# Optimization experiments

Hardware: AMD Instinct MI355X
Metric: run time of the kernel (lower is better)

## Reference

```python
import jax, jax.numpy as jnp
import numpy as np
from jax import lax

E = 1024      # embed_dim
H = 16        # num_heads
HD = E // H   # head_dim = 64
GS = 2        # head_group_size
G = H // GS   # num head groups = 8
KQ = 3        # kq kernel q size
KK = 3        # kq kernel k size


def setup_inputs() -> dict:
    key = jax.random.key(0)
    ks = jax.random.split(key, 18)
    B, S = 2, 1024
    def rn(k, shape, scale=1.0):
        return jax.random.normal(k, shape, dtype=jnp.float32) * scale
    return {
        "Q": rn(ks[0], (B, S, E)),
        "K": rn(ks[1], (B, S, E)),
        "V": rn(ks[2], (B, S, E)),
        "Wq": rn(ks[3], (E, E), 0.02), "bq": rn(ks[4], (E,), 0.02),
        "Wk": rn(ks[5], (E, E), 0.02), "bk": rn(ks[6], (E,), 0.02),
        "Wv": rn(ks[7], (E, E), 0.02), "bv": rn(ks[8], (E,), 0.02),
        "Wo": rn(ks[9], (E, E), 0.02), "bo": rn(ks[10], (E,), 0.02),
        # depthwise key-query conv: [out=H, in/groups=1, KQ, KK]
        "kq_w": rn(ks[11], (H, 1, KQ, KK), 0.1),
        "kq_b": rn(ks[12], (H,), 0.02),
        # grouped 1x1 head-mix conv: weight [H, GS] (kernel dim squeezed), bias [H]
        "mix_w": rn(ks[13], (H, GS), 0.3),
        "mix_b": rn(ks[14], (H,), 0.02),
        # DynamicTanh params over head_dim (channels_last)
        "dyt_alpha": jnp.array([0.5], dtype=jnp.float32),
        "dyt_w": jnp.ones((HD,), dtype=jnp.float32),
        "dyt_b": jnp.zeros((HD,), dtype=jnp.float32),
        "depth_scale": jnp.ones((1,), dtype=jnp.float32),
    }


def reference(Q, K, V, Wq, bq, Wk, bk, Wv, bv, Wo, bo,
              kq_w, kq_b, mix_w, mix_b, dyt_alpha, dyt_w, dyt_b, depth_scale):
    B, S, _ = Q.shape
    scale = HD ** (-0.5)
    # projections -> [B, H, S, HD]
    q = (Q @ Wq + bq).reshape(B, S, H, HD).transpose(0, 2, 1, 3)
    k = (K @ Wk + bk).reshape(B, S, H, HD).transpose(0, 2, 1, 3)
    v = (V @ Wv + bv).reshape(B, S, H, HD).transpose(0, 2, 1, 3)

    # raw logits [B, H, Sq, Sk], multiplicative causal mask (zeros above diag)
    logits = jnp.einsum('bhqd,bhkd->bhqk', q, k) * scale
    causal = jnp.tril(jnp.ones((S, S), dtype=logits.dtype))
    logits = logits * causal

    # per-head (depthwise) key-query conv2d; torch pads q-dim by 2 both sides
    # then crops to first S rows (causal in q), k-dim padded symmetrically by 1
    conv = lax.conv_general_dilated(
        logits, kq_w, window_strides=(1, 1),
        padding=[(KQ - 1, KQ - 1), ((KK - 1) // 2, (KK - 1) // 2)],
        dimension_numbers=('NCHW', 'OIHW', 'NCHW'),
        feature_group_count=H)
    conv = conv + kq_b[None, :, None, None]
    conv = conv[:, :, :S, :]

    attn = jax.nn.softmax(conv, axis=-1)

    # grouped 1x1 head-mixing conv (within groups of GS heads) + bias
    attn_g = attn.reshape(B, G, GS, S, S)
    mw = mix_w.reshape(G, GS, GS)  # [group, out_in_group, in_in_group]
    mixed = jnp.einsum('goj,bgjqk->bgoqk', mw, attn_g).reshape(B, H, S, S)
    mixed = mixed + mix_b[None, :, None, None]

    out = jnp.einsum('bhqk,bhkd->bhqd', mixed, v)
    # DynamicTanh over head_dim (channels_last) + depth scale
    out = jnp.tanh(dyt_alpha * out) * dyt_w + dyt_b
    out = out * depth_scale
    out = out.transpose(0, 2, 1, 3).reshape(B, S, E)
    return out @ Wo + bo
```

## Files before the change

### kernel.cpp

```cpp
#include <hip/hip_runtime.h>
#include <cstdint>
#include <cstddef>

typedef __bf16 bf16;
typedef __bf16 bf16x8 __attribute__((ext_vector_type(8)));
typedef float f32x4 __attribute__((ext_vector_type(4)));

#define DEVI static __device__ __forceinline__

DEVI unsigned int cvt_pk_bf16(float lo, float hi) {
  unsigned int bl = __float_as_uint(lo);
  bl += 0x7fffu + ((bl >> 16) & 1u);
  unsigned int bh = __float_as_uint(hi);
  bh += 0x7fffu + ((bh >> 16) & 1u);
  return (bl >> 16) | (bh & 0xffff0000u);
}
DEVI float bf_lo(unsigned int u) { return __uint_as_float(u << 16); }
DEVI float bf_hi(unsigned int u) { return __uint_as_float(u & 0xffff0000u); }

DEVI void gload16(const bf16* g, bf16* l) {
  __builtin_amdgcn_global_load_lds(
      (const __attribute__((address_space(1))) unsigned int*)g,
      (__attribute__((address_space(3))) unsigned int*)l, 16, 0, 0);
}

__global__ __launch_bounds__(256) void wtr_k(
    const float* __restrict__ Wq, const float* __restrict__ Wk,
    const float* __restrict__ Wv, const float* __restrict__ Wo,
    bf16* __restrict__ Wt)
{
  const int z = blockIdx.z;
  const float* W = (z == 0) ? Wq : (z == 1) ? Wk : (z == 2) ? Wv : Wo;
  bf16* out = Wt + ((size_t)z << 20);
  const int n0 = blockIdx.x * 64, k0 = blockIdx.y * 64;
  __shared__ bf16 Ts[64 * 72];
  const int tid = threadIdx.x;
  #pragma unroll
  for (int i = 0; i < 4; ++i) {
    int t = tid + i * 256;
    int kr = t >> 4, nc = t & 15;
    float4 v = *(const float4*)(W + (size_t)(k0 + kr) * 1024 + n0 + nc * 4);
    Ts[(nc * 4 + 0) * 72 + kr] = (bf16)v.x;
    Ts[(nc * 4 + 1) * 72 + kr] = (bf16)v.y;
    Ts[(nc * 4 + 2) * 72 + kr] = (bf16)v.z;
    Ts[(nc * 4 + 3) * 72 + kr] = (bf16)v.w;
  }
  __syncthreads();
  const int n = tid >> 2, kc = tid & 3;
  *(uint4*)(out + (size_t)(n0 + n) * 1024 + k0 + kc * 16) =
      *(const uint4*)(&Ts[n * 72 + kc * 16]);
  *(uint4*)(out + (size_t)(n0 + n) * 1024 + k0 + kc * 16 + 8) =
      *(const uint4*)(&Ts[n * 72 + kc * 16 + 8]);
}

__global__ __launch_bounds__(256) void a2bf_k(
    const float* __restrict__ Q, const float* __restrict__ K,
    const float* __restrict__ V, bf16* __restrict__ Ab)
{
  const int z = blockIdx.y;
  const float* A = (z == 0) ? Q : (z == 1) ? K : V;
  bf16* o = Ab + ((size_t)z << 21);
  const int idx = blockIdx.x * 256 + threadIdx.x;
  const float4 v0 = *(const float4*)(A + (size_t)idx * 8);
  const float4 v1 = *(const float4*)(A + (size_t)idx * 8 + 4);
  uint4 u;
  u.x = cvt_pk_bf16(v0.x, v0.y);
  u.y = cvt_pk_bf16(v0.z, v0.w);
  u.z = cvt_pk_bf16(v1.x, v1.y);
  u.w = cvt_pk_bf16(v1.z, v1.w);
  *(uint4*)(o + (size_t)idx * 8) = u;
}

__global__ __launch_bounds__(256) void proj_gemm_k(
    const bf16* __restrict__ Ab, const bf16* __restrict__ Wt,
    const float* __restrict__ bq, const float* __restrict__ bk,
    const float* __restrict__ bv, bf16* __restrict__ outbase)
{
  const int z = blockIdx.z;
  const bf16* A  = Ab + ((size_t)z << 21);
  const bf16* Bt = Wt + ((size_t)z << 20);
  const float* bias = (z == 0) ? bq : (z == 1) ? bk : bv;
  bf16* outb = outbase + ((size_t)z << 21);

  __shared__ __align__(16) bf16 As[2][4096];
  __shared__ __align__(16) bf16 Bs[2][2048];

  const int tid = threadIdx.x, lane = tid & 63, wid = tid >> 6;
  const int q4 = lane >> 4, n16 = lane & 15;
  const int wm = wid >> 1, wn = wid & 1;
  const int bid = blockIdx.x;
  const int m0 = (bid & 15) * 128, n0 = (bid >> 4) * 64;

  const int cA0 = wid * 64 + lane, cA1 = cA0 + 256;
  const bf16* gA0 = A + (size_t)(m0 + (cA0 >> 2)) * 1024 + (((cA0 & 3) ^ ((cA0 >> 3) & 3)) << 3);
  const bf16* gA1 = A + (size_t)(m0 + (cA1 >> 2)) * 1024 + (((cA1 & 3) ^ ((cA1 >> 3) & 3)) << 3);
  const bf16* gB  = Bt + (size_t)(n0 + (cA0 >> 2)) * 1024 + (((cA0 & 3) ^ ((cA0 >> 3) & 3)) << 3);
  const int qsw = (q4 ^ ((n16 >> 1) & 3)) << 4;

  f32x4 acc[4][2] = {};

  gload16(gA0, &As[0][wid * 512]);
  gload16(gA1, &As[0][2048 + wid * 512]);
  gload16(gB,  &Bs[0][wid * 512]);
  __syncthreads();

  int cur = 0;
  for (int kb = 0; kb < 32; ++kb) {
    if (kb < 31) {
      const int kc = (kb + 1) * 32;
      gload16(gA0 + kc, &As[cur ^ 1][wid * 512]);
      gload16(gA1 + kc, &As[cur ^ 1][2048 + wid * 512]);
      gload16(gB + kc,  &Bs[cur ^ 1][wid * 512]);
    }
    const char* ab = (const char*)&As[cur][0];
    const char* bb = (const char*)&Bs[cur][0];
    bf16x8 af[4], bfv[2];
    #pragma unroll
    for (int rt = 0; rt < 4; ++rt)
      af[rt] = *(const bf16x8*)(ab + (wm * 64 + rt * 16 + n16) * 64 + qsw);
    #pragma unroll
    for (int ct = 0; ct < 2; ++ct)
      bfv[ct] = *(const bf16x8*)(bb + (wn * 32 + ct * 16 + n16) * 64 + qsw);
    #pragma unroll
    for (int rt = 0; rt < 4; ++rt)
      #pragma unroll
      for (int ct = 0; ct < 2; ++ct)
        acc[rt][ct] = __builtin_amdgcn_mfma_f32_16x16x32_bf16(af[rt], bfv[ct], acc[rt][ct], 0, 0, 0);
    __syncthreads();
    cur ^= 1;
  }

  if (z < 2) {
    const int h = n0 >> 6;
    #pragma unroll
    for (int ct = 0; ct < 2; ++ct) {
      const int dl = wn * 32 + ct * 16 + n16;
      const float bvl = bias[n0 + dl];
      #pragma unroll
      for (int rt = 0; rt < 4; ++rt) {
        #pragma unroll
        for (int r = 0; r < 4; ++r) {
          int row = m0 + wm * 64 + rt * 16 + q4 * 4 + r;
          int b2 = row >> 10, s = row & 1023;
          outb[((size_t)((b2 * 16 + h) * 1024 + s) << 6) + dl] =
              (bf16)(acc[rt][ct][r] + bvl);
        }
      }
    }
  } else {
    const int b2 = m0 >> 10, kt0 = (m0 & 1023) >> 6, hh = n0 >> 6;
    bf16* vout = outb + ((size_t)(b2 * 16 + hh) << 16) + (size_t)(kt0 + wm) * 4096;
    #pragma unroll
    for (int rt = 0; rt < 4; ++rt) {
      const int kk = rt >> 1;
      const int q4c = (rt & 1) * 2 + (q4 >> 1);
      const int jo = (q4 & 1) * 4;
      #pragma unroll
      for (int ct = 0; ct < 2; ++ct) {
        const int cl = wn * 32 + ct * 16 + n16;
        const float bvl = bias[n0 + cl];
        unsigned int p0 = cvt_pk_bf16(acc[rt][ct][0] + bvl, acc[rt][ct][1] + bvl);
        unsigned int p1 = cvt_pk_bf16(acc[rt][ct][2] + bvl, acc[rt][ct][3] + bvl);
        *(uint2*)(vout + kk * 2048 + (wn * 2 + ct) * 512 + (q4c * 16 + n16) * 8 + jo) =
            make_uint2(p0, p1);
      }
    }
  }
}

__global__ __launch_bounds__(256) void out_gemm_k(
    const bf16* __restrict__ Ab, const bf16* __restrict__ Bt,
    const float* __restrict__ bias, float* __restrict__ outf)
{
  __shared__ __align__(16) bf16 As[2][2048];
  __shared__ __align__(16) bf16 Bs[2][2048];
  const int tid = threadIdx.x, lane = tid & 63, wid = tid >> 6;
  const int q4 = lane >> 4, n16 = lane & 15;
  const int wm = wid >> 1, wn = wid & 1;
  const int bid = blockIdx.x;
  const int m0 = (bid & 31) * 64, n0 = (bid >> 5) * 64;
  const int c = wid * 64 + lane;
  const bf16* gA = Ab + (size_t)(m0 + (c >> 2)) * 1024 + (((c & 3) ^ ((c >> 3) & 3)) << 3);
  const bf16* gB = Bt + (size_t)(n0 + (c >> 2)) * 1024 + (((c & 3) ^ ((c >> 3) & 3)) << 3);
  const int qsw = (q4 ^ ((n16 >> 1) & 3)) << 4;
  f32x4 acc[2][2] = {};

  gload16(gA, &As[0][wid * 512]);
  gload16(gB, &Bs[0][wid * 512]);
  __syncthreads();

  int cur = 0;
  for (int kb = 0; kb < 32; ++kb) {
    if (kb < 31) {
      const int kc = (kb + 1) * 32;
      gload16(gA + kc, &As[cur ^ 1][wid * 512]);
      gload16(gB + kc, &Bs[cur ^ 1][wid * 512]);
    }
    const char* ab = (const char*)&As[cur][0];
    const char* bb = (const char*)&Bs[cur][0];
    bf16x8 af[2], bfv[2];
    #pragma unroll
    for (int rt = 0; rt < 2; ++rt)
      af[rt] = *(const bf16x8*)(ab + (wm * 32 + rt * 16 + n16) * 64 + qsw);
    #pragma unroll
    for (int ct = 0; ct < 2; ++ct)
      bfv[ct] = *(const bf16x8*)(bb + (wn * 32 + ct * 16 + n16) * 64 + qsw);
    #pragma unroll
    for (int rt = 0; rt < 2; ++rt)
      #pragma unroll
      for (int ct = 0; ct < 2; ++ct)
        acc[rt][ct] = __builtin_amdgcn_mfma_f32_16x16x32_bf16(af[rt], bfv[ct], acc[rt][ct], 0, 0, 0);
    __syncthreads();
    cur ^= 1;
  }
  #pragma unroll
  for (int ct = 0; ct < 2; ++ct) {
    int col = n0 + wn * 32 + ct * 16 + n16;
    float bvl = bias[col];
    #pragma unroll
    for (int rt = 0; rt < 2; ++rt)
      #pragma unroll
      for (int r = 0; r < 4; ++r) {
        int row = m0 + wm * 32 + rt * 16 + q4 * 4 + r;
        outf[(size_t)row * 1024 + col] = acc[rt][ct][r] + bvl;
      }
  }
}

__global__ void vtile_sum_k(const bf16* __restrict__ V2, float* __restrict__ Tsum)
{
  int kt = blockIdx.x, h = blockIdx.y, b = blockIdx.z, d = threadIdx.x;
  int ctt = d >> 4, n16c = d & 15;
  const bf16* p = V2 + ((size_t)(b * 16 + h) << 16) + kt * 4096 + ctt * 512 + n16c * 8;
  float s = 0.f;
  #pragma unroll
  for (int kk = 0; kk < 2; ++kk)
    #pragma unroll
    for (int q4i = 0; q4i < 4; ++q4i)
      #pragma unroll
      for (int j = 0; j < 8; ++j)
        s += (float)p[kk * 2048 + q4i * 128 + j];
  Tsum[((b * 16 + h) * 16 + kt) * 64 + d] = s;
}

__global__ void vtail_k(const float* __restrict__ Tsum, float* __restrict__ Vtail)
{
  int h = blockIdx.x, b = blockIdx.y, d = threadIdx.x;
  float c = 0.f;
  Vtail[((b * 16 + h) * 17 + 16) * 64 + d] = 0.f;
  for (int kt = 15; kt >= 0; --kt) {
    c += Tsum[((b * 16 + h) * 16 + kt) * 64 + d];
    Vtail[((b * 16 + h) * 17 + kt) * 64 + d] = c;
  }
}

__global__ __launch_bounds__(320) void logits_conv_k(
    const bf16* __restrict__ qh, const bf16* __restrict__ kh,
    const float* __restrict__ kq_w, const float* __restrict__ kq_b,
    bf16* __restrict__ conv_out, float* __restrict__ tstats)
{
  const int tt = blockIdx.x;
  int qt = 0, base = 0;
  while (qt < 15 && base + qt + 2 <= tt) { base += qt + 2; ++qt; }
  const int ct = tt - base;
  const int h = blockIdx.y, b = blockIdx.z;
  const int q0 = qt * 64, c0 = ct * 64;
  __shared__ __align__(16) char un[18432];
  bf16* Kst = (bf16*)un;
  float* Ls = (float*)un;
  const int tid = threadIdx.x;
  const int lane = tid & 63, wid = tid >> 6;
  const int q4 = lane >> 4, n16 = lane & 15;
  const bf16* qb = qh + ((size_t)(b * 16 + h) << 16);
  const bf16* kb = kh + ((size_t)(b * 16 + h) << 16);

  const int ar = min(max(q0 - 2 + wid * 16 + n16, 0), 1023);
  bf16x8 a0 = *(const bf16x8*)(qb + ar * 64 + q4 * 8);
  bf16x8 a1 = *(const bf16x8*)(qb + ar * 64 + 32 + q4 * 8);

  for (int t = tid; t < 640; t += 320) {
    int row = t >> 3, ch = t & 7;
    int br = min(max(c0 - 1 + row, 0), 1023);
    *(uint4*)(&Kst[row * 72 + ch * 8]) = *(const uint4*)(kb + br * 64 + ch * 8);
  }
  __syncthreads();

  f32x4 acc[5] = {};
  #pragma unroll
  for (int c5 = 0; c5 < 5; ++c5) {
    int brow = c5 * 16 + n16;
    bf16x8 b0 = *(const bf16x8*)(&Kst[brow * 72 + q4 * 8]);
    bf16x8 b1 = *(const bf16x8*)(&Kst[brow * 72 + 32 + q4 * 8]);
    acc[c5] = __builtin_amdgcn_mfma_f32_16x16x32_bf16(a0, b0, acc[c5], 0, 0, 0);
    acc[c5] = __builtin_amdgcn_mfma_f32_16x16x32_bf16(a1, b1, acc[c5], 0, 0, 0);
  }
  __syncthreads();

  #pragma unroll
  for (int c5 = 0; c5 < 5; ++c5) {
    #pragma unroll
    for (int r = 0; r < 4; ++r) {
      int Lrow = wid * 16 + q4 * 4 + r;
      int Lcol = c5 * 16 + n16;
      if (Lrow < 66 && Lcol < 66) {
        int rg = q0 - 2 + Lrow;
        int cg = c0 - 1 + Lcol;
        float v = (cg >= 0 && cg <= rg) ? acc[c5][r] * 0.125f : 0.f;
        Ls[Lrow * 68 + Lcol] = v;
      }
    }
  }
  __syncthreads();

  if (tid < 256) {
    float w9[9];
    #pragma unroll
    for (int i = 0; i < 9; ++i) w9[i] = kq_w[h * 9 + i];
    const float bb = kq_b[h];
    const size_t tplane = (size_t)(b * 16 + h) * 151 + base + ct;
    bf16* tb = conv_out + tplane * 4096;
    float2* st = (float2*)tstats + tplane * 64;

    const int r = tid >> 2, qr = tid & 3;
    float4 R0[5], R1[5], R2[5];
    const float* L0 = &Ls[r * 68 + qr * 16];
    #pragma unroll
    for (int i = 0; i < 5; ++i) {
      R0[i] = *(const float4*)(L0 + i * 4);
      R1[i] = *(const float4*)(L0 + 68 + i * 4);
      R2[i] = *(const float4*)(L0 + 136 + i * 4);
    }
    const float* f0 = (const float*)R0;
    const float* f1 = (const float*)R1;
    const float* f2 = (const float*)R2;
    float o[16];
    #pragma unroll
    for (int jj = 0; jj < 16; ++jj)
      o[jj] = bb + w9[0]*f0[jj] + w9[1]*f0[jj+1] + w9[2]*f0[jj+2]
                 + w9[3]*f1[jj] + w9[4]*f1[jj+1] + w9[5]*f1[jj+2]
                 + w9[6]*f2[jj] + w9[7]*f2[jj+1] + w9[8]*f2[jj+2];
    float mx = o[0];
    #pragma unroll
    for (int jj = 1; jj < 16; ++jj) mx = fmaxf(mx, o[jj]);
    mx = fmaxf(mx, __shfl_xor(mx, 1));
    mx = fmaxf(mx, __shfl_xor(mx, 2));
    unsigned int p[8];
    #pragma unroll
    for (int jj = 0; jj < 8; ++jj)
      p[jj] = cvt_pk_bf16(__expf(o[2*jj] - mx), __expf(o[2*jj+1] - mx));
    const int kk = qr >> 1, q4b = (qr & 1) * 2, sr = r >> 4, n16r = r & 15;
    *(uint4*)(tb + (sr * 2 + kk) * 512 + (q4b * 16 + n16r) * 8)       = *(const uint4*)&p[0];
    *(uint4*)(tb + (sr * 2 + kk) * 512 + ((q4b + 1) * 16 + n16r) * 8) = *(const uint4*)&p[4];
    float s = 0.f;
    #pragma unroll
    for (int jj = 0; jj < 8; ++jj) s += bf_lo(p[jj]) + bf_hi(p[jj]);
    s += __shfl_xor(s, 1);
    s += __shfl_xor(s, 2);
    if (qr == 0) st[r] = make_float2(mx, s);
  }
}

__global__ __launch_bounds__(256) void combine_k(
    const float* __restrict__ tstats, const float* __restrict__ kq_b,
    float* __restrict__ rs)
{
  const int ridx = blockIdx.x * 256 + threadIdx.x;
  const int q = ridx & 1023, h = (ridx >> 10) & 15, plane = ridx >> 10;
  const int qt = q >> 6;
  const int nkt = min(qt + 2, 16);
  const int Tc = 1024 - (nkt << 6);
  const float2* ts = (const float2*)tstats +
      ((size_t)plane * 151 + (size_t)(qt * (qt + 3) / 2)) * 64 + (q & 63);
  const float kb = kq_b[h];
  float mx = (Tc > 0) ? kb : -3.0e38f;
  for (int kt = 0; kt < nkt; ++kt) mx = fmaxf(mx, ts[(size_t)kt * 64].x);
  float s = (float)Tc * __expf(kb - mx);
  for (int kt = 0; kt < nkt; ++kt) {
    float2 v = ts[(size_t)kt * 64];
    s += v.y * __expf(v.x - mx);
  }
  rs[(size_t)ridx * 2]     = mx;
  rs[(size_t)ridx * 2 + 1] = 1.f / s;
}

__global__ __launch_bounds__(256) void pv_k(
    const bf16* __restrict__ conv_out, const bf16* __restrict__ V2,
    const float* __restrict__ rs, const float* __restrict__ tstats,
    const float* __restrict__ Vtail,
    const float* __restrict__ mix_w, const float* __restrict__ mix_b,
    const float* __restrict__ kq_b,
    const float* __restrict__ dyt_alpha, const float* __restrict__ dyt_w,
    const float* __restrict__ dyt_b, const float* __restrict__ depth_scale,
    bf16* __restrict__ out_attn)
{
  const int qt16 = blockIdx.x, g = blockIdx.y, b = blockIdx.z;
  const int qt = qt16 >> 2;
  const int nkt = min(qt + 2, 16);
  const int Tc = 1024 - (nkt << 6);
  const int tid = threadIdx.x, lane = tid & 63, wid = tid >> 6;
  const int q4 = lane >> 4, n16 = lane & 15;
  const int oo = wid >> 1, kh = wid & 1;
  const int h0 = 2 * g, ho = h0 + oo;
  const int sr = qt16 & 3, strow = sr * 16;
  const size_t tbase = (size_t)(qt * (qt + 3) / 2);

  const int qrow = qt16 * 16 + n16;
  const float2 r0 = *(const float2*)(rs + ((((size_t)(b * 16 + h0)     << 10) + qrow) << 1));
  const float2 r1 = *(const float2*)(rs + ((((size_t)(b * 16 + h0 + 1) << 10) + qrow) << 1));
  const float m0 = r0.x, m1 = r1.x;
  const float mwa = mix_w[ho * 2 + 0], mwb = mix_w[ho * 2 + 1];
  const float wa = mwa * r0.y, wb = mwb * r1.y;

  const bf16* pb0 = conv_out +
      ((size_t)(b * 16 + h0) * 151 + tbase) * 4096 + sr * 1024 + lane * 8;
  const bf16* pb1 = pb0 + (size_t)151 * 4096;
  const float2* ts0 = (const float2*)tstats +
      ((size_t)(b * 16 + h0) * 151 + tbase) * 64 + strow + n16;
  const float2* ts1 = ts0 + (size_t)151 * 64;
  const bf16* vb = V2 + ((size_t)(b * 16 + ho) << 16) + lane * 8;

  const int niter = (nkt - kh + 1) >> 1;
  float wk0[8], wk1[8];
  #pragma unroll
  for (int i = 0; i < 8; ++i) {
    int ktc = (i < niter) ? (kh + 2 * i) : 0;
    wk0[i] = wa * __expf(ts0[(size_t)ktc * 64].x - m0);
    wk1[i] = wb * __expf(ts1[(size_t)ktc * 64].x - m1);
  }

  f32x4 acc[4] = {};
  int ii = 0;
  for (int kt = kh; kt < nkt; kt += 2, ++ii) {
    uint4 u0[2], u1[2];
    #pragma unroll
    for (int kk = 0; kk < 2; ++kk) {
      u0[kk] = *(const uint4*)(pb0 + (size_t)kt * 4096 + kk * 512);
      u1[kk] = *(const uint4*)(pb1 + (size_t)kt * 4096 + kk * 512);
    }
    bf16x8 bv[2][4];
    #pragma unroll
    for (int kk = 0; kk < 2; ++kk)
      #pragma unroll
      for (int ctt = 0; ctt < 4; ++ctt)
        bv[kk][ctt] = *(const bf16x8*)(vb + (size_t)kt * 4096 + kk * 2048 + ctt * 512);
    const float w0 = wk0[ii], w1 = wk1[ii];
    #pragma unroll
    for (int kk = 0; kk < 2; ++kk) {
      bf16x8 af;
      const unsigned int* a0p = (const unsigned int*)&u0[kk];
      const unsigned int* a1p = (const unsigned int*)&u1[kk];
      #pragma unroll
      for (int i2 = 0; i2 < 4; ++i2) {
        float a0 = w0 * bf_lo(a0p[i2]) + w1 * bf_lo(a1p[i2]);
        float a1 = w0 * bf_hi(a0p[i2]) + w1 * bf_hi(a1p[i2]);
        ((unsigned int*)&af)[i2] = cvt_pk_bf16(a0, a1);
      }
      #pragma unroll
      for (int ctt = 0; ctt < 4; ++ctt)
        acc[ctt] = __builtin_amdgcn_mfma_f32_16x16x32_bf16(af, bv[kk][ctt], acc[ctt], 0, 0, 0);
    }
  }

  __shared__ float Pp[2][16][64];
  if (kh == 1) {
    #pragma unroll
    for (int ctt = 0; ctt < 4; ++ctt)
      #pragma unroll
      for (int r = 0; r < 4; ++r)
        Pp[oo][q4 * 4 + r][ctt * 16 + n16] = acc[ctt][r];
  }
  __syncthreads();
  if (kh == 1) return;
  #pragma unroll
  for (int ctt = 0; ctt < 4; ++ctt)
    #pragma unroll
    for (int r = 0; r < 4; ++r)
      acc[ctt][r] += Pp[oo][q4 * 4 + r][ctt * 16 + n16];

  const float kqb0 = kq_b[h0], kqb1 = kq_b[h0 + 1];
  float tw[4];
  #pragma unroll
  for (int r = 0; r < 4; ++r) {
    int qr = qt16 * 16 + q4 * 4 + r;
    float2 s0 = *(const float2*)(rs + ((((size_t)(b * 16 + h0)     << 10) + qr) << 1));
    float2 s1 = *(const float2*)(rs + ((((size_t)(b * 16 + h0 + 1) << 10) + qr) << 1));
    tw[r] = (Tc > 0) ? (mwa * s0.y * __expf(kqb0 - s0.x) +
                        mwb * s1.y * __expf(kqb1 - s1.x)) : 0.f;
  }
  const float mb = mix_b[ho];
  const float alpha = dyt_alpha[0], dsc = depth_scale[0];
  const float* vt = Vtail + (size_t)(b * 16 + ho) * 17 * 64;
  #pragma unroll
  for (int ctt = 0; ctt < 4; ++ctt) {
    int d = ctt * 16 + n16;
    float vtn = vt[(size_t)nkt * 64 + d];
    float vt0 = vt[d];
    float wgt = dyt_w[d], bds = dyt_b[d];
    #pragma unroll
    for (int r = 0; r < 4; ++r) {
      float v = acc[ctt][r] + tw[r] * vtn + mb * vt0;
      float e = __expf(2.f * alpha * v);
      float th = 1.f - 2.f / (e + 1.f);
      float y = (th * wgt + bds) * dsc;
      int qr = qt16 * 16 + q4 * 4 + r;
      out_attn[(((size_t)(b * 1024 + qr)) << 10) + ho * 64 + d] = (bf16)y;
    }
  }
}

extern "C" void kernel_launch(void* const* d_in, const int* in_sizes, int n_in,
                              void* d_out, int out_size, void* d_ws, size_t ws_size,
                              hipStream_t stream) {
  const float* Q    = (const float*)d_in[0];
  const float* Kx   = (const float*)d_in[1];
  const float* V    = (const float*)d_in[2];
  const float* Wq   = (const float*)d_in[3];
  const float* bq   = (const float*)d_in[4];
  const float* Wk   = (const float*)d_in[5];
  const float* bk   = (const float*)d_in[6];
  const float* Wv   = (const float*)d_in[7];
  const float* bv   = (const float*)d_in[8];
  const float* Wo   = (const float*)d_in[9];
  const float* bo   = (const float*)d_in[10];
  const float* kq_w = (const float*)d_in[11];
  const float* kq_b = (const float*)d_in[12];
  const float* mixw = (const float*)d_in[13];
  const float* mixb = (const float*)d_in[14];
  const float* dyta = (const float*)d_in[15];
  const float* dytw = (const float*)d_in[16];
  const float* dytb = (const float*)d_in[17];
  const float* dsc  = (const float*)d_in[18];

  char* ws = (char*)d_ws;
  bf16* qh     = (bf16*)(ws);
  float* tstat = (float*)(ws + (size_t)(12 << 20));
  float* Vtail = (float*)(ws + (size_t)(16 << 20));
  float* Tsum  = (float*)(ws + (size_t)(16 << 20) + (256 << 10));
  float* rsbuf = (float*)(ws + (size_t)(16 << 20) + (512 << 10));
  bf16* WtT    = (bf16*)(ws + (size_t)(17 << 20));
  bf16* oat    = (bf16*)(ws + (size_t)(17 << 20));
  bf16* conv   = (bf16*)(ws + (size_t)(25 << 20));
  bf16* Ab     = (bf16*)(ws + (size_t)(25 << 20));
  bf16* kh     = qh + ((size_t)1 << 21);
  bf16* V2     = qh + ((size_t)2 << 21);

  wtr_k<<<dim3(16, 16, 4), 256, 0, stream>>>(Wq, Wk, Wv, Wo, WtT);
  a2bf_k<<<dim3(1024, 3), 256, 0, stream>>>(Q, Kx, V, Ab);
  proj_gemm_k<<<dim3(256, 1, 3), 256, 0, stream>>>(Ab, WtT, bq, bk, bv, qh);
  vtile_sum_k<<<dim3(16, 16, 2), 64, 0, stream>>>(V2, Tsum);
  vtail_k<<<dim3(16, 2), 64, 0, stream>>>(Tsum, Vtail);
  logits_conv_k<<<dim3(151, 16, 2), 320, 0, stream>>>(qh, kh, kq_w, kq_b, conv, tstat);
  combine_k<<<dim3(128), 256, 0, stream>>>(tstat, kq_b, rsbuf);
  pv_k<<<dim3(64, 8, 2), 256, 0, stream>>>(conv, V2, rsbuf, tstat, Vtail, mixw, mixb, kq_b,
                                           dyta, dytw, dytb, dsc, oat);
  out_gemm_k<<<dim3(512), 256, 0, stream>>>(oat, WtT + ((size_t)3 << 20), bo, (float*)d_out);
}
```

Baseline: 218.6 us.

## Merge prep kernels, fold combine into pv, double GEMM K-tile, pad LDS stride

Merges the weight-transpose and activation-conversion kernels into one launch, merges the V tile-sum and suffix-sum kernels, and moves the softmax row-statistics combine into pv_k using shared memory. This cuts the launch count from nine to six and drops two global scratch round trips. The projection and output GEMMs now use a 64-wide K tile with an 8-way XOR swizzle, which halves the loop iterations and barriers at the cost of twice the LDS. The logits_conv LDS row stride goes from 68 to 72. The serial vsum_k running in only 32 blocks and the combine work repeated in every pv_k block could add latency.

```diff
diff --git a/kernel.cpp b/kernel.cpp
--- a/kernel.cpp
+++ b/kernel.cpp
@@ -24,51 +24,51 @@
       (__attribute__((address_space(3))) unsigned int*)l, 16, 0, 0);
 }
 
-__global__ __launch_bounds__(256) void wtr_k(
+__global__ __launch_bounds__(256) void prep_k(
     const float* __restrict__ Wq, const float* __restrict__ Wk,
     const float* __restrict__ Wv, const float* __restrict__ Wo,
-    bf16* __restrict__ Wt)
+    const float* __restrict__ Q, const float* __restrict__ K,
+    const float* __restrict__ V, bf16* __restrict__ Wt,
+    bf16* __restrict__ Ab)
 {
-  const int z = blockIdx.z;
-  const float* W = (z == 0) ? Wq : (z == 1) ? Wk : (z == 2) ? Wv : Wo;
-  bf16* out = Wt + ((size_t)z << 20);
-  const int n0 = blockIdx.x * 64, k0 = blockIdx.y * 64;
   __shared__ bf16 Ts[64 * 72];
-  const int tid = threadIdx.x;
-  #pragma unroll
-  for (int i = 0; i < 4; ++i) {
-    int t = tid + i * 256;
-    int kr = t >> 4, nc = t & 15;
-    float4 v = *(const float4*)(W + (size_t)(k0 + kr) * 1024 + n0 + nc * 4);
-    Ts[(nc * 4 + 0) * 72 + kr] = (bf16)v.x;
-    Ts[(nc * 4 + 1) * 72 + kr] = (bf16)v.y;
-    Ts[(nc * 4 + 2) * 72 + kr] = (bf16)v.z;
-    Ts[(nc * 4 + 3) * 72 + kr] = (bf16)v.w;
-  }
-  __syncthreads();
-  const int n = tid >> 2, kc = tid & 3;
-  *(uint4*)(out + (size_t)(n0 + n) * 1024 + k0 + kc * 16) =
-      *(const uint4*)(&Ts[n * 72 + kc * 16]);
-  *(uint4*)(out + (size_t)(n0 + n) * 1024 + k0 + kc * 16 + 8) =
-      *(const uint4*)(&Ts[n * 72 + kc * 16 + 8]);
-}
-
-__global__ __launch_bounds__(256) void a2bf_k(
-    const float* __restrict__ Q, const float* __restrict__ K,
-    const float* __restrict__ V, bf16* __restrict__ Ab)
-{
-  const int z = blockIdx.y;
-  const float* A = (z == 0) ? Q : (z == 1) ? K : V;
-  bf16* o = Ab + ((size_t)z << 21);
-  const int idx = blockIdx.x * 256 + threadIdx.x;
-  const float4 v0 = *(const float4*)(A + (size_t)idx * 8);
-  const float4 v1 = *(const float4*)(A + (size_t)idx * 8 + 4);
-  uint4 u;
-  u.x = cvt_pk_bf16(v0.x, v0.y);
-  u.y = cvt_pk_bf16(v0.z, v0.w);
-  u.z = cvt_pk_bf16(v1.x, v1.y);
-  u.w = cvt_pk_bf16(v1.z, v1.w);
-  *(uint4*)(o + (size_t)idx * 8) = u;
+  const int bid = blockIdx.x, tid = threadIdx.x;
+  if (bid < 1024) {
+    const int z = bid >> 8;
+    const float* W = (z == 0) ? Wq : (z == 1) ? Wk : (z == 2) ? Wv : Wo;
+    bf16* out = Wt + ((size_t)z << 20);
+    const int n0 = (bid & 15) * 64, k0 = ((bid >> 4) & 15) * 64;
+    #pragma unroll
+    for (int i = 0; i < 4; ++i) {
+      int t = tid + i * 256;
+      int kr = t >> 4, nc = t & 15;
+      float4 v = *(const float4*)(W + (size_t)(k0 + kr) * 1024 + n0 + nc * 4);
+      Ts[(nc * 4 + 0) * 72 + kr] = (bf16)v.x;
+      Ts[(nc * 4 + 1) * 72 + kr] = (bf16)v.y;
+      Ts[(nc * 4 + 2) * 72 + kr] = (bf16)v.z;
+      Ts[(nc * 4 + 3) * 72 + kr] = (bf16)v.w;
+    }
+    __syncthreads();
+    const int n = tid >> 2, kc = tid & 3;
+    *(uint4*)(out + (size_t)(n0 + n) * 1024 + k0 + kc * 16) =
+        *(const uint4*)(&Ts[n * 72 + kc * 16]);
+    *(uint4*)(out + (size_t)(n0 + n) * 1024 + k0 + kc * 16 + 8) =
+        *(const uint4*)(&Ts[n * 72 + kc * 16 + 8]);
+  } else {
+    const int t = bid - 1024;
+    const int z = t >> 10, x = t & 1023;
+    const float* A = (z == 0) ? Q : (z == 1) ? K : V;
+    bf16* o = Ab + ((size_t)z << 21);
+    const size_t idx = (size_t)x * 256 + tid;
+    const float4 v0 = *(const float4*)(A + idx * 8);
+    const float4 v1 = *(const float4*)(A + idx * 8 + 4);
+    uint4 u;
+    u.x = cvt_pk_bf16(v0.x, v0.y);
+    u.y = cvt_pk_bf16(v0.z, v0.w);
+    u.z = cvt_pk_bf16(v1.x, v1.y);
+    u.w = cvt_pk_bf16(v1.z, v1.w);
+    *(uint4*)(o + idx * 8) = u;
+  }
 }
 
 __global__ __launch_bounds__(256) void proj_gemm_k(
@@ -82,8 +82,8 @@
   const float* bias = (z == 0) ? bq : (z == 1) ? bk : bv;
   bf16* outb = outbase + ((size_t)z << 21);
 
-  __shared__ __align__(16) bf16 As[2][4096];
-  __shared__ __align__(16) bf16 Bs[2][2048];
+  __shared__ __align__(16) bf16 Asm[2][8192];
+  __shared__ __align__(16) bf16 Bsm[2][4096];
 
   const int tid = threadIdx.x, lane = tid & 63, wid = tid >> 6;
   const int q4 = lane >> 4, n16 = lane & 15;
@@ -91,41 +91,59 @@
   const int bid = blockIdx.x;
   const int m0 = (bid & 15) * 128, n0 = (bid >> 4) * 64;
 
-  const int cA0 = wid * 64 + lane, cA1 = cA0 + 256;
-  const bf16* gA0 = A + (size_t)(m0 + (cA0 >> 2)) * 1024 + (((cA0 & 3) ^ ((cA0 >> 3) & 3)) << 3);
-  const bf16* gA1 = A + (size_t)(m0 + (cA1 >> 2)) * 1024 + (((cA1 & 3) ^ ((cA1 >> 3) & 3)) << 3);
-  const bf16* gB  = Bt + (size_t)(n0 + (cA0 >> 2)) * 1024 + (((cA0 & 3) ^ ((cA0 >> 3) & 3)) << 3);
-  const int qsw = (q4 ^ ((n16 >> 1) & 3)) << 4;
+  const int cbase = wid * 64 + lane;
+  const bf16* gA[4];
+  #pragma unroll
+  for (int i = 0; i < 4; ++i) {
+    int cc = cbase + i * 256;
+    gA[i] = A + (size_t)(m0 + (cc >> 3)) * 1024 + (((cc & 7) ^ ((cc >> 3) & 7)) << 3);
+  }
+  const bf16* gB[2];
+  #pragma unroll
+  for (int i = 0; i < 2; ++i) {
+    int cc = cbase + i * 256;
+    gB[i] = Bt + (size_t)(n0 + (cc >> 3)) * 1024 + (((cc & 7) ^ ((cc >> 3) & 7)) << 3);
+  }
+  const int swl = n16 & 7;
 
   f32x4 acc[4][2] = {};
 
-  gload16(gA0, &As[0][wid * 512]);
-  gload16(gA1, &As[0][2048 + wid * 512]);
-  gload16(gB,  &Bs[0][wid * 512]);
+  #pragma unroll
+  for (int i = 0; i < 4; ++i) gload16(gA[i], &Asm[0][i * 2048 + wid * 512]);
+  #pragma unroll
+  for (int i = 0; i < 2; ++i) gload16(gB[i], &Bsm[0][i * 2048 + wid * 512]);
   __syncthreads();
 
   int cur = 0;
-  for (int kb = 0; kb < 32; ++kb) {
-    if (kb < 31) {
-      const int kc = (kb + 1) * 32;
-      gload16(gA0 + kc, &As[cur ^ 1][wid * 512]);
-      gload16(gA1 + kc, &As[cur ^ 1][2048 + wid * 512]);
-      gload16(gB + kc,  &Bs[cur ^ 1][wid * 512]);
-    }
-    const char* ab = (const char*)&As[cur][0];
-    const char* bb = (const char*)&Bs[cur][0];
-    bf16x8 af[4], bfv[2];
-    #pragma unroll
-    for (int rt = 0; rt < 4; ++rt)
-      af[rt] = *(const bf16x8*)(ab + (wm * 64 + rt * 16 + n16) * 64 + qsw);
-    #pragma unroll
-    for (int ct = 0; ct < 2; ++ct)
-      bfv[ct] = *(const bf16x8*)(bb + (wn * 32 + ct * 16 + n16) * 64 + qsw);
-    #pragma unroll
-    for (int rt = 0; rt < 4; ++rt)
+  for (int t = 0; t < 16; ++t) {
+    if (t < 15) {
+      const int kc = (t + 1) * 64;
+      #pragma unroll
+      for (int i = 0; i < 4; ++i) gload16(gA[i] + kc, &Asm[cur ^ 1][i * 2048 + wid * 512]);
+      #pragma unroll
+      for (int i = 0; i < 2; ++i) gload16(gB[i] + kc, &Bsm[cur ^ 1][i * 2048 + wid * 512]);
+    }
+    const char* ab = (const char*)&Asm[cur][0];
+    const char* bb = (const char*)&Bsm[cur][0];
+    bf16x8 af[2][4], bfv[2][2];
+    #pragma unroll
+    for (int kk2 = 0; kk2 < 2; ++kk2) {
+      #pragma unroll
+      for (int rt = 0; rt < 4; ++rt)
+        af[kk2][rt] = *(const bf16x8*)(ab + (wm * 64 + rt * 16 + n16) * 128 +
+                                       (((kk2 * 4 + q4) ^ swl) << 4));
       #pragma unroll
       for (int ct = 0; ct < 2; ++ct)
-        acc[rt][ct] = __builtin_amdgcn_mfma_f32_16x16x32_bf16(af[rt], bfv[ct], acc[rt][ct], 0, 0, 0);
+        bfv[kk2][ct] = *(const bf16x8*)(bb + (wn * 32 + ct * 16 + n16) * 128 +
+                                        (((kk2 * 4 + q4) ^ swl) << 4));
+    }
+    #pragma unroll
+    for (int kk2 = 0; kk2 < 2; ++kk2)
+      #pragma unroll
+      for (int rt = 0; rt < 4; ++rt)
+        #pragma unroll
+        for (int ct = 0; ct < 2; ++ct)
+          acc[rt][ct] = __builtin_amdgcn_mfma_f32_16x16x32_bf16(af[kk2][rt], bfv[kk2][ct], acc[rt][ct], 0, 0, 0);
     __syncthreads();
     cur ^= 1;
   }
@@ -172,44 +190,63 @@
     const bf16* __restrict__ Ab, const bf16* __restrict__ Bt,
     const float* __restrict__ bias, float* __restrict__ outf)
 {
-  __shared__ __align__(16) bf16 As[2][2048];
-  __shared__ __align__(16) bf16 Bs[2][2048];
+  __shared__ __align__(16) bf16 Asm[2][4096];
+  __shared__ __align__(16) bf16 Bsm[2][4096];
   const int tid = threadIdx.x, lane = tid & 63, wid = tid >> 6;
   const int q4 = lane >> 4, n16 = lane & 15;
   const int wm = wid >> 1, wn = wid & 1;
   const int bid = blockIdx.x;
   const int m0 = (bid & 31) * 64, n0 = (bid >> 5) * 64;
-  const int c = wid * 64 + lane;
-  const bf16* gA = Ab + (size_t)(m0 + (c >> 2)) * 1024 + (((c & 3) ^ ((c >> 3) & 3)) << 3);
-  const bf16* gB = Bt + (size_t)(n0 + (c >> 2)) * 1024 + (((c & 3) ^ ((c >> 3) & 3)) << 3);
-  const int qsw = (q4 ^ ((n16 >> 1) & 3)) << 4;
+  const int cbase = wid * 64 + lane;
+  const bf16* gA[2];
+  const bf16* gB[2];
+  #pragma unroll
+  for (int i = 0; i < 2; ++i) {
+    int cc = cbase + i * 256;
+    gA[i] = Ab + (size_t)(m0 + (cc >> 3)) * 1024 + (((cc & 7) ^ ((cc >> 3) & 7)) << 3);
+    gB[i] = Bt + (size_t)(n0 + (cc >> 3)) * 1024 + (((cc & 7) ^ ((cc >> 3) & 7)) << 3);
+  }
+  const int swl = n16 & 7;
   f32x4 acc[2][2] = {};
 
-  gload16(gA, &As[0][wid * 512]);
-  gload16(gB, &Bs[0][wid * 512]);
+  #pragma unroll
+  for (int i = 0; i < 2; ++i) {
+    gload16(gA[i], &Asm[0][i * 2048 + wid * 512]);
+    gload16(gB[i], &Bsm[0][i * 2048 + wid * 512]);
+  }
   __syncthreads();
 
   int cur = 0;
-  for (int kb = 0; kb < 32; ++kb) {
-    if (kb < 31) {
-      const int kc = (kb + 1) * 32;
-      gload16(gA + kc, &As[cur ^ 1][wid * 512]);
-      gload16(gB + kc, &Bs[cur ^ 1][wid * 512]);
-    }
-    const char* ab = (const char*)&As[cur][0];
-    const char* bb = (const char*)&Bs[cur][0];
-    bf16x8 af[2], bfv[2];
-    #pragma unroll
-    for (int rt = 0; rt < 2; ++rt)
-      af[rt] = *(const bf16x8*)(ab + (wm * 32 + rt * 16 + n16) * 64 + qsw);
-    #pragma unroll
-    for (int ct = 0; ct < 2; ++ct)
-      bfv[ct] = *(const bf16x8*)(bb + (wn * 32 + ct * 16 + n16) * 64 + qsw);
-    #pragma unroll
-    for (int rt = 0; rt < 2; ++rt)
+  for (int t = 0; t < 16; ++t) {
+    if (t < 15) {
+      const int kc = (t + 1) * 64;
+      #pragma unroll
+      for (int i = 0; i < 2; ++i) {
+        gload16(gA[i] + kc, &Asm[cur ^ 1][i * 2048 + wid * 512]);
+        gload16(gB[i] + kc, &Bsm[cur ^ 1][i * 2048 + wid * 512]);
+      }
+    }
+    const char* ab = (const char*)&Asm[cur][0];
+    const char* bb = (const char*)&Bsm[cur][0];
+    bf16x8 af[2][2], bfv[2][2];
+    #pragma unroll
+    for (int kk2 = 0; kk2 < 2; ++kk2) {
+      #pragma unroll
+      for (int rt = 0; rt < 2; ++rt)
+        af[kk2][rt] = *(const bf16x8*)(ab + (wm * 32 + rt * 16 + n16) * 128 +
+                                       (((kk2 * 4 + q4) ^ swl) << 4));
       #pragma unroll
       for (int ct = 0; ct < 2; ++ct)
-        acc[rt][ct] = __builtin_amdgcn_mfma_f32_16x16x32_bf16(af[rt], bfv[ct], acc[rt][ct], 0, 0, 0);
+        bfv[kk2][ct] = *(const bf16x8*)(bb + (wn * 32 + ct * 16 + n16) * 128 +
+                                        (((kk2 * 4 + q4) ^ swl) << 4));
+    }
+    #pragma unroll
+    for (int kk2 = 0; kk2 < 2; ++kk2)
+      #pragma unroll
+      for (int rt = 0; rt < 2; ++rt)
+        #pragma unroll
+        for (int ct = 0; ct < 2; ++ct)
+          acc[rt][ct] = __builtin_amdgcn_mfma_f32_16x16x32_bf16(af[kk2][rt], bfv[kk2][ct], acc[rt][ct], 0, 0, 0);
     __syncthreads();
     cur ^= 1;
   }
@@ -227,30 +264,29 @@
   }
 }
 
-__global__ void vtile_sum_k(const bf16* __restrict__ V2, float* __restrict__ Tsum)
+__global__ void vsum_k(const bf16* __restrict__ V2, float* __restrict__ Vtail)
 {
-  int kt = blockIdx.x, h = blockIdx.y, b = blockIdx.z, d = threadIdx.x;
-  int ctt = d >> 4, n16c = d & 15;
-  const bf16* p = V2 + ((size_t)(b * 16 + h) << 16) + kt * 4096 + ctt * 512 + n16c * 8;
-  float s = 0.f;
-  #pragma unroll
-  for (int kk = 0; kk < 2; ++kk)
-    #pragma unroll
-    for (int q4i = 0; q4i < 4; ++q4i)
-      #pragma unroll
-      for (int j = 0; j < 8; ++j)
-        s += (float)p[kk * 2048 + q4i * 128 + j];
-  Tsum[((b * 16 + h) * 16 + kt) * 64 + d] = s;
-}
-
-__global__ void vtail_k(const float* __restrict__ Tsum, float* __restrict__ Vtail)
-{
-  int h = blockIdx.x, b = blockIdx.y, d = threadIdx.x;
+  const int h = blockIdx.x, b = blockIdx.y, d = threadIdx.x;
+  const int ctt = d >> 4, n16c = d & 15;
+  const bf16* p = V2 + ((size_t)(b * 16 + h) << 16) + ctt * 512 + n16c * 8;
+  float ts[16];
+  for (int kt = 0; kt < 16; ++kt) {
+    float s = 0.f;
+    #pragma unroll
+    for (int kk = 0; kk < 2; ++kk)
+      #pragma unroll
+      for (int q4i = 0; q4i < 4; ++q4i)
+        #pragma unroll
+        for (int j = 0; j < 8; ++j)
+          s += (float)p[kt * 4096 + kk * 2048 + q4i * 128 + j];
+    ts[kt] = s;
+  }
+  float* vt = Vtail + (size_t)(b * 16 + h) * 17 * 64;
+  vt[16 * 64 + d] = 0.f;
   float c = 0.f;
-  Vtail[((b * 16 + h) * 17 + 16) * 64 + d] = 0.f;
   for (int kt = 15; kt >= 0; --kt) {
-    c += Tsum[((b * 16 + h) * 16 + kt) * 64 + d];
-    Vtail[((b * 16 + h) * 17 + kt) * 64 + d] = c;
+    c += ts[kt];
+    vt[kt * 64 + d] = c;
   }
 }
 
@@ -265,7 +301,7 @@
   const int ct = tt - base;
   const int h = blockIdx.y, b = blockIdx.z;
   const int q0 = qt * 64, c0 = ct * 64;
-  __shared__ __align__(16) char un[18432];
+  __shared__ __align__(16) char un[19456];
   bf16* Kst = (bf16*)un;
   float* Ls = (float*)un;
   const int tid = threadIdx.x;
@@ -306,7 +342,7 @@
         int rg = q0 - 2 + Lrow;
         int cg = c0 - 1 + Lcol;
         float v = (cg >= 0 && cg <= rg) ? acc[c5][r] * 0.125f : 0.f;
-        Ls[Lrow * 68 + Lcol] = v;
+        Ls[Lrow * 72 + Lcol] = v;
       }
     }
   }
@@ -323,12 +359,12 @@
 
     const int r = tid >> 2, qr = tid & 3;
     float4 R0[5], R1[5], R2[5];
-    const float* L0 = &Ls[r * 68 + qr * 16];
+    const float* L0 = &Ls[r * 72 + qr * 16];
     #pragma unroll
     for (int i = 0; i < 5; ++i) {
       R0[i] = *(const float4*)(L0 + i * 4);
-      R1[i] = *(const float4*)(L0 + 68 + i * 4);
-      R2[i] = *(const float4*)(L0 + 136 + i * 4);
+      R1[i] = *(const float4*)(L0 + 72 + i * 4);
+      R2[i] = *(const float4*)(L0 + 144 + i * 4);
     }
     const float* f0 = (const float*)R0;
     const float* f1 = (const float*)R1;
@@ -360,33 +396,9 @@
   }
 }
 
-__global__ __launch_bounds__(256) void combine_k(
-    const float* __restrict__ tstats, const float* __restrict__ kq_b,
-    float* __restrict__ rs)
-{
-  const int ridx = blockIdx.x * 256 + threadIdx.x;
-  const int q = ridx & 1023, h = (ridx >> 10) & 15, plane = ridx >> 10;
-  const int qt = q >> 6;
-  const int nkt = min(qt + 2, 16);
-  const int Tc = 1024 - (nkt << 6);
-  const float2* ts = (const float2*)tstats +
-      ((size_t)plane * 151 + (size_t)(qt * (qt + 3) / 2)) * 64 + (q & 63);
-  const float kb = kq_b[h];
-  float mx = (Tc > 0) ? kb : -3.0e38f;
-  for (int kt = 0; kt < nkt; ++kt) mx = fmaxf(mx, ts[(size_t)kt * 64].x);
-  float s = (float)Tc * __expf(kb - mx);
-  for (int kt = 0; kt < nkt; ++kt) {
-    float2 v = ts[(size_t)kt * 64];
-    s += v.y * __expf(v.x - mx);
-  }
-  rs[(size_t)ridx * 2]     = mx;
-  rs[(size_t)ridx * 2 + 1] = 1.f / s;
-}
-
 __global__ __launch_bounds__(256) void pv_k(
     const bf16* __restrict__ conv_out, const bf16* __restrict__ V2,
-    const float* __restrict__ rs, const float* __restrict__ tstats,
-    const float* __restrict__ Vtail,
+    const float* __restrict__ tstats, const float* __restrict__ Vtail,
     const float* __restrict__ mix_w, const float* __restrict__ mix_b,
     const float* __restrict__ kq_b,
     const float* __restrict__ dyt_alpha, const float* __restrict__ dyt_w,
@@ -404,9 +416,25 @@
   const int sr = qt16 & 3, strow = sr * 16;
   const size_t tbase = (size_t)(qt * (qt + 3) / 2);
 
-  const int qrow = qt16 * 16 + n16;
-  const float2 r0 = *(const float2*)(rs + ((((size_t)(b * 16 + h0)     << 10) + qrow) << 1));
-  const float2 r1 = *(const float2*)(rs + ((((size_t)(b * 16 + h0 + 1) << 10) + qrow) << 1));
+  __shared__ float2 rsS[2][16];
+  if (tid < 32) {
+    const int hh = tid >> 4, rw = tid & 15;
+    const float2* tsp = (const float2*)tstats +
+        ((size_t)(b * 16 + h0 + hh) * 151 + tbase) * 64 + strow + rw;
+    const float kb2 = kq_b[h0 + hh];
+    float mx = (Tc > 0) ? kb2 : -3.0e38f;
+    for (int kt = 0; kt < nkt; ++kt) mx = fmaxf(mx, tsp[(size_t)kt * 64].x);
+    float s = (float)Tc * __expf(kb2 - mx);
+    for (int kt = 0; kt < nkt; ++kt) {
+      float2 v = tsp[(size_t)kt * 64];
+      s += v.y * __expf(v.x - mx);
+    }
+    rsS[hh][rw] = make_float2(mx, 1.f / s);
+  }
+  __syncthreads();
+
+  const float2 r0 = rsS[0][n16];
+  const float2 r1 = rsS[1][n16];
   const float m0 = r0.x, m1 = r1.x;
   const float mwa = mix_w[ho * 2 + 0], mwb = mix_w[ho * 2 + 1];
   const float wa = mwa * r0.y, wb = mwb * r1.y;
@@ -481,9 +509,8 @@
   float tw[4];
   #pragma unroll
   for (int r = 0; r < 4; ++r) {
-    int qr = qt16 * 16 + q4 * 4 + r;
-    float2 s0 = *(const float2*)(rs + ((((size_t)(b * 16 + h0)     << 10) + qr) << 1));
-    float2 s1 = *(const float2*)(rs + ((((size_t)(b * 16 + h0 + 1) << 10) + qr) << 1));
+    float2 s0 = rsS[0][q4 * 4 + r];
+    float2 s1 = rsS[1][q4 * 4 + r];
     tw[r] = (Tc > 0) ? (mwa * s0.y * __expf(kqb0 - s0.x) +
                         mwb * s1.y * __expf(kqb1 - s1.x)) : 0.f;
   }
@@ -535,8 +562,6 @@
   bf16* qh     = (bf16*)(ws);
   float* tstat = (float*)(ws + (size_t)(12 << 20));
   float* Vtail = (float*)(ws + (size_t)(16 << 20));
-  float* Tsum  = (float*)(ws + (size_t)(16 << 20) + (256 << 10));
-  float* rsbuf = (float*)(ws + (size_t)(16 << 20) + (512 << 10));
   bf16* WtT    = (bf16*)(ws + (size_t)(17 << 20));
   bf16* oat    = (bf16*)(ws + (size_t)(17 << 20));
   bf16* conv   = (bf16*)(ws + (size_t)(25 << 20));
@@ -544,14 +569,11 @@
   bf16* kh     = qh + ((size_t)1 << 21);
   bf16* V2     = qh + ((size_t)2 << 21);
 
-  wtr_k<<<dim3(16, 16, 4), 256, 0, stream>>>(Wq, Wk, Wv, Wo, WtT);
-  a2bf_k<<<dim3(1024, 3), 256, 0, stream>>>(Q, Kx, V, Ab);
+  prep_k<<<dim3(4096), 256, 0, stream>>>(Wq, Wk, Wv, Wo, Q, Kx, V, WtT, Ab);
   proj_gemm_k<<<dim3(256, 1, 3), 256, 0, stream>>>(Ab, WtT, bq, bk, bv, qh);
-  vtile_sum_k<<<dim3(16, 16, 2), 64, 0, stream>>>(V2, Tsum);
-  vtail_k<<<dim3(16, 2), 64, 0, stream>>>(Tsum, Vtail);
+  vsum_k<<<dim3(16, 2), 64, 0, stream>>>(V2, Vtail);
   logits_conv_k<<<dim3(151, 16, 2), 320, 0, stream>>>(qh, kh, kq_w, kq_b, conv, tstat);
-  combine_k<<<dim3(128), 256, 0, stream>>>(tstat, kq_b, rsbuf);
-  pv_k<<<dim3(64, 8, 2), 256, 0, stream>>>(conv, V2, rsbuf, tstat, Vtail, mixw, mixb, kq_b,
+  pv_k<<<dim3(64, 8, 2), 256, 0, stream>>>(conv, V2, tstat, Vtail, mixw, mixb, kq_b,
                                            dyta, dytw, dytb, dsc, oat);
   out_gemm_k<<<dim3(512), 256, 0, stream>>>(oat, WtT + ((size_t)3 << 20), bo, (float*)d_out);
 }
```

After: 212.6 us. 2.7% less time.
